# Performance work log

Hardware: AMD Instinct MI355X
Metric: run time of the kernel (lower is better)

## Reference

```python
import jax, jax.numpy as jnp
import numpy as np

N, D, H, C, E = 50000, 128, 4, 32, 600000  # C = D // H
LRELU_SLOPE = 0.2
EPS_LN = 1e-5
EPS_SOFTMAX = 1e-16


def layer_norm(x, g, b):
    m = jnp.mean(x, axis=-1, keepdims=True)
    v = jnp.mean((x - m) ** 2, axis=-1, keepdims=True)
    return (x - m) * jax.lax.rsqrt(v + EPS_LN) * g + b


def setup_inputs() -> dict:
    key = jax.random.key(0)
    ks = jax.random.split(key, 10)
    glorot = lambda k, shape: jax.random.normal(k, shape, jnp.float32) * np.sqrt(2.0 / (shape[0] + shape[-1]))
    return {
        "x": jax.random.normal(ks[0], (N, D), jnp.float32),
        "edge_index": jax.random.randint(ks[1], (2, E), 0, N, jnp.int32),
        "edge_attr": jax.random.uniform(ks[2], (E,), jnp.float32),
        "timestamps": jax.random.uniform(ks[3], (E,), jnp.float32),
        "W_gat": glorot(ks[4], (D, H * C)),
        "att_src": glorot(ks[5], (H, C)),
        "att_dst": glorot(ks[6], (H, C)),
        "bias_gat": jnp.zeros((H * C,), jnp.float32),
        "ln1_g": jnp.ones((D,), jnp.float32),
        "ln1_b": jnp.zeros((D,), jnp.float32),
        "ln2_g": jnp.ones((D,), jnp.float32),
        "ln2_b": jnp.zeros((D,), jnp.float32),
    }


def reference(x, edge_index, edge_attr, timestamps, W_gat, att_src, att_dst,
              bias_gat, ln1_g, ln1_b, ln2_g, ln2_b):
    n = x.shape[0]
    # TemporalAttention is just LayerNorm(x)
    xt = layer_norm(x, ln1_g, ln1_b)

    # GATConv with default add_self_loops=True, concat=True, dropout=0 (eval)
    loop = jnp.arange(n, dtype=edge_index.dtype)
    src = jnp.concatenate([edge_index[0], loop])  # [E+N]
    dst = jnp.concatenate([edge_index[1], loop])  # aggregation target

    h = (xt @ W_gat).reshape(n, H, C)            # [N,H,C]
    a_src = jnp.sum(h * att_src, axis=-1)        # [N,H]
    a_dst = jnp.sum(h * att_dst, axis=-1)        # [N,H]

    alpha = jax.nn.leaky_relu(a_src[src] + a_dst[dst], LRELU_SLOPE)  # [E+N,H]
    amax = jax.ops.segment_max(alpha, dst, num_segments=n)
    alpha = jnp.exp(alpha - amax[dst])
    asum = jax.ops.segment_sum(alpha, dst, num_segments=n)
    alpha = alpha / (asum[dst] + EPS_SOFTMAX)

    msg = h[src] * alpha[:, :, None]             # [E+N,H,C]
    out = jax.ops.segment_sum(msg, dst, num_segments=n).reshape(n, H * C) + bias_gat

    # residual + LayerNorm (dropout is identity in eval)
    return layer_norm(xt + out, ln2_g, ln2_b)
```

## Files before the change

### kernel.cpp

```cpp
#include <hip/hip_runtime.h>
#include <hip/hip_bf16.h>

typedef unsigned short u16;
typedef unsigned int u32;
typedef __attribute__((ext_vector_type(8))) short short8;
typedef __attribute__((ext_vector_type(4))) float f32x4;

#define LRELU_SLOPE 0.2f
#define EPS_LN 1e-5f
#define EPS_SM 1e-16f
#define SCAN_CHUNK 4096
#define NBLK 256

__device__ __forceinline__ float bflo(u32 u){ union{u32 i; float f;} x; x.i = u<<16; return x.f; }
__device__ __forceinline__ float bfhi(u32 u){ union{u32 i; float f;} x; x.i = u & 0xffff0000u; return x.f; }
__device__ __forceinline__ float bf1(u16 u){ union{u32 i; float f;} x; x.i = ((u32)u)<<16; return x.f; }
__device__ __forceinline__ u16 f2bf(float f){
  union{float f; u32 i;} x; x.f=f; u32 i=x.i;
  u32 r = (i + 0x7fffu + ((i>>16)&1u))>>16; return (u16)r;
}
__device__ __forceinline__ u32 pack2(float a, float b){ return (u32)f2bf(a) | ((u32)f2bf(b)<<16); }
__device__ __forceinline__ float lrelu(float x){ return x > 0.f ? x : LRELU_SLOPE*x; }

__device__ __forceinline__ float wsum(float v){
  #pragma unroll
  for(int o=32;o>0;o>>=1) v += __shfl_xor(v,o,64);
  return v;
}

__global__ __launch_bounds__(256) void ln1A_kernel(const float* __restrict__ x,
    const float* __restrict__ g, const float* __restrict__ b,
    u16* __restrict__ xt, int n,
    const int* __restrict__ edst, int* __restrict__ bhT, int E, int CH, int NB){
  __shared__ u32 hist[512];
  int tid = threadIdx.x;
  bool doA = blockIdx.x < NBLK;
  if(doA){ for(int bb=tid; bb<NB; bb+=256) hist[bb]=0u; }

  int row  = blockIdx.x*4 + (tid>>6);
  int lane = tid & 63;
  if(row < n){
    float2 xv = ((const float2*)(x + (size_t)row*128))[lane];
    float v0 = xv.x, v1 = xv.y;
    float mean = wsum(v0+v1) * (1.f/128.f);
    float d0 = v0-mean, d1 = v1-mean;
    float var = wsum(d0*d0 + d1*d1) * (1.f/128.f);
    float rstd = rsqrtf(var + EPS_LN);
    float2 gv = ((const float2*)g)[lane], bv = ((const float2*)b)[lane];
    float o0 = d0*rstd*gv.x + bv.x;
    float o1 = d1*rstd*gv.y + bv.y;
    ((u32*)(xt + (size_t)row*128))[lane] = pack2(o0, o1);
  }
  if(doA){
    __syncthreads();
    int i = blockIdx.x;
    int e0=i*CH, e1=min(E, e0+CH);
    for(int e=e0+tid; e<e1; e+=256) atomicAdd(&hist[(u32)edst[e]>>7], 1u);
    __syncthreads();
    for(int bb=tid; bb<NB; bb+=256) bhT[bb*NBLK + i] = (int)hist[bb];
  }
}

__global__ __launch_bounds__(256) void scanA_kernel(const int* __restrict__ deg,
    int* __restrict__ pref, int* __restrict__ bsum, int n){
  __shared__ int part[256];
  int tid = threadIdx.x;
  int base = blockIdx.x*SCAN_CHUNK + tid*16;
  int v[16]; int s=0;
  #pragma unroll
  for(int i=0;i<16;i++){ int idx=base+i; int xv=(idx<n)? deg[idx]:0; v[i]=s; s+=xv; }
  part[tid]=s; __syncthreads();
  int mys=s;
  for(int off=1;off<256;off<<=1){
    int t = (tid>=off)? part[tid-off] : 0;
    __syncthreads(); part[tid]+=t; __syncthreads();
  }
  int run = part[tid]-mys;
  #pragma unroll
  for(int i=0;i<16;i++){
    int idx=base+i;
    if(idx<=n) pref[idx]=v[i]+run;
  }
  if(tid==255) bsum[blockIdx.x]=part[255];
}

__global__ __launch_bounds__(256) void binC_kernel(const int* __restrict__ src,
    const int* __restrict__ dst, const int* __restrict__ bhpref, const int* __restrict__ bsum2,
    u32* __restrict__ ebuf, int E, int CH, int NB, int nb2){
  __shared__ u32 cur[512];
  __shared__ int boff[64];
  int tid = threadIdx.x, i = blockIdx.x;
  if(tid<64){
    int v = (tid<nb2)? bsum2[tid] : 0;
    int inc = v;
    #pragma unroll
    for(int o=1;o<64;o<<=1){ int t=__shfl_up(inc,o,64); if(tid>=o) inc+=t; }
    boff[tid] = inc - v;
  }
  __syncthreads();
  for(int bb=tid; bb<NB; bb+=256){
    int j = bb*NBLK + i;
    cur[bb] = (u32)(bhpref[j] + boff[j>>12]);
  }
  __syncthreads();
  int e0=i*CH, e1=min(E, e0+CH);
  for(int e=e0+tid; e<e1; e+=256){
    u32 s = (u32)src[e], d = (u32)dst[e];
    u32 pos = atomicAdd(&cur[d>>7], 1u);
    ebuf[pos] = s | ((d & 127u) << 16);
  }
}

__global__ __launch_bounds__(256) void gemmD_kernel(const u16* __restrict__ xt,
    const float* __restrict__ W, const float* __restrict__ att_src, const float* __restrict__ att_dst,
    u16* __restrict__ h, float* __restrict__ a_src, float* __restrict__ a_dst, int n,
    const u32* __restrict__ ebuf, const int* __restrict__ bhpref, const int* __restrict__ bsum2,
    int* __restrict__ rowptr, u16* __restrict__ col, int NB, int nb2, int E){
  __shared__ u16 Wf[16384];
  __shared__ u16 Xb[64*136];
  __shared__ int dcnt[128], dcur[128], dboff[64];
  int tid = threadIdx.x;

  if(blockIdx.x < (u32)NB){
    int bkt = blockIdx.x;
    if(tid<64){
      int v = (tid<nb2)? bsum2[tid] : 0;
      int inc = v;
      #pragma unroll
      for(int o=1;o<64;o<<=1){ int t=__shfl_up(inc,o,64); if(tid>=o) inc+=t; }
      dboff[tid] = inc - v;
    }
    if(tid<128) dcnt[tid]=0;
    __syncthreads();
    int j0 = bkt*NBLK, j1 = (bkt+1)*NBLK;
    int base = bhpref[j0] + dboff[j0>>12];
    int end  = bhpref[j1] + dboff[j1>>12];
    int cb = end - base;
    for(int k=tid; k<cb; k+=256) atomicAdd(&dcnt[(ebuf[base+k]>>16)&127], 1);
    __syncthreads();
    for(int o=1;o<128;o<<=1){
      int t = (tid>=o && tid<128)? dcnt[tid-o] : 0;
      __syncthreads();
      if(tid<128) dcnt[tid]+=t;
      __syncthreads();
    }
    int nd = min(128, n - (bkt<<7));
    if(tid<128){
      int excl = tid? dcnt[tid-1] : 0;
      dcur[tid] = excl;
      if(tid<nd) rowptr[(bkt<<7)+tid] = base + excl;
    }
    if(bkt==0 && tid==0) rowptr[n] = E;
    __syncthreads();
    for(int k=tid; k<cb; k+=256){
      u32 v = ebuf[base+k];
      int l = (int)((v>>16)&127u);
      int p = atomicAdd(&dcur[l], 1);
      col[base+p] = (u16)(v & 0xffffu);
    }
  }

  int r0 = blockIdx.x*64;
  const float4* W4 = (const float4*)W;
  for(int p=tid; p<2048; p+=256){
    int g = p & 31, kk = p >> 5;
    int k0 = kk*2, n0 = g*4;
    float4 w0 = W4[k0*32 + g];
    float4 w1 = W4[(k0+1)*32 + g];
    int ks = k0>>5, q = (k0>>3)&3, j = k0&7;
    float e0[4] = {w0.x,w0.y,w0.z,w0.w};
    float e1[4] = {w1.x,w1.y,w1.z,w1.w};
    #pragma unroll
    for(int u=0;u<4;u++){
      int nn = n0+u;
      int idx = (((nn>>4)*4 + ks)*64 + q*16 + (nn&15))*8 + j;
      ((u32*)Wf)[idx>>1] = pack2(e0[u], e1[u]);
    }
  }
  for(int i=tid; i<1024; i+=256){
    int row = i>>4, seg = i&15;
    int gr = r0+row;
    uint4 v = (gr<n) ? ((const uint4*)(xt + (size_t)gr*128))[seg] : make_uint4(0,0,0,0);
    *(uint4*)&Xb[row*136 + seg*8] = v;
  }
  __syncthreads();

  int w = tid>>6, lane = tid&63;
  int slab = w*16, c = lane&15, q = lane>>4;
  f32x4 acc[8];
  #pragma unroll
  for(int t=0;t<8;t++) acc[t] = (f32x4){0.f,0.f,0.f,0.f};
  #pragma unroll
  for(int ks=0;ks<4;ks++){
    short8 A = *(const short8*)&Xb[(slab + c)*136 + ks*32 + q*8];
    #pragma unroll
    for(int t=0;t<8;t++){
      short8 B = *(const short8*)&Wf[((t*4+ks)*64 + lane)*8];
      acc[t] = __builtin_amdgcn_mfma_f32_16x16x32_bf16(A, B, acc[t], 0, 0, 0);
    }
  }
  __syncthreads();
  #pragma unroll
  for(int t=0;t<8;t++){
    #pragma unroll
    for(int r=0;r<4;r++){
      Xb[(slab + q*4 + r)*136 + t*16 + c] = f2bf(acc[t][r]);
    }
  }
  __syncthreads();
  {
    int row = tid>>2, qt = tid&3;
    int gr = r0+row;
    if(gr<n){
      const uint4* src = (const uint4*)((const char*)Xb + row*272 + qt*64);
      uint4* dst = (uint4*)((char*)(h + (size_t)gr*128) + qt*64);
      dst[0] = src[0];
      dst[1] = src[1];
      dst[2] = src[2];
      dst[3] = src[3];
    }
    int hd = qt;
    if(gr<n){
      float as=0.f, ad=0.f;
      const u16* hp = &Xb[row*136 + hd*32];
      #pragma unroll
      for(int sgm=0;sgm<4;sgm++){
        #pragma unroll
        for(int e=0;e<8;e++){
          float v = bf1(hp[sgm*8+e]);
          as = fmaf(v, att_src[hd*32+sgm*8+e], as);
          ad = fmaf(v, att_dst[hd*32+sgm*8+e], ad);
        }
      }
      a_src[(size_t)gr*4+hd] = as;
      a_dst[(size_t)gr*4+hd] = ad;
    }
  }
}

__global__ __launch_bounds__(256) void agg_kernel(const u16* __restrict__ h,
    const float* __restrict__ a_src, const float* __restrict__ a_dst,
    const int* __restrict__ rowptr, const u16* __restrict__ col,
    const u16* __restrict__ xt, const float* __restrict__ bias,
    const float* __restrict__ g2, const float* __restrict__ b2,
    float* __restrict__ out, int n){
  __shared__ float ybuf[16*68];
  __shared__ int   sxbuf[16*17];
  int lane = threadIdx.x & 63;
  int wv   = threadIdx.x >> 6;
  int g    = lane >> 4;
  int li   = lane & 15;
  int hc   = li >> 2;
  int gid  = wv*4 + g;
  float* yb = ybuf  + gid*68;
  int*   sb = sxbuf + gid*17;
  int d    = blockIdx.x*16 + gid;
  bool dok = d < n;
  int dc   = dok ? d : (n-1);

  float4 ad  = ((const float4*)a_dst)[dc];
  float4 asd = ((const float4*)a_src)[dc];
  float ad_h = hc==0? ad.x  : hc==1? ad.y  : hc==2? ad.z  : ad.w;
  float as_h = hc==0? asd.x : hc==1? asd.y : hc==2? asd.z : asd.w;
  float t_h  = __expf(fminf(lrelu(as_h + ad_h), 60.f));

  int base = rowptr[dc];
  int deg  = dok ? (rowptr[dc+1] - base) : 0;
  int dm = deg;
  dm = max(dm, __shfl_xor(dm, 16, 64));
  dm = max(dm, __shfl_xor(dm, 32, 64));

  float p0=0.f,p1=0.f,p2=0.f,p3=0.f;
  float acc[8]={};
  for(int j0=0;j0<dm;j0+=16){
    int j = j0 + li;
    bool vv = j < deg;
    int sx = vv ? (int)col[base+j] : 0;
    float4 a = ((const float4*)a_src)[sx];
    float y0 = vv ? __expf(fminf(lrelu(a.x+ad.x),60.f)) : 0.f;
    float y1 = vv ? __expf(fminf(lrelu(a.y+ad.y),60.f)) : 0.f;
    float y2 = vv ? __expf(fminf(lrelu(a.z+ad.z),60.f)) : 0.f;
    float y3 = vv ? __expf(fminf(lrelu(a.w+ad.w),60.f)) : 0.f;
    p0+=y0; p1+=y1; p2+=y2; p3+=y3;
    *(float4*)&yb[li*4] = make_float4(y0,y1,y2,y3);
    sb[li] = sx;
    __builtin_amdgcn_sched_barrier(0);
    int ccm = min(deg - j0, 16);
    for(int jj=0; jj<ccm; jj++){
      float al = yb[jj*4 + hc];
      int   sj = sb[jj];
      uint4 hv = *(const uint4*)(h + (size_t)sj*128 + li*8);
      acc[0]=fmaf(al,bflo(hv.x),acc[0]); acc[1]=fmaf(al,bfhi(hv.x),acc[1]);
      acc[2]=fmaf(al,bflo(hv.y),acc[2]); acc[3]=fmaf(al,bfhi(hv.y),acc[3]);
      acc[4]=fmaf(al,bflo(hv.z),acc[4]); acc[5]=fmaf(al,bfhi(hv.z),acc[5]);
      acc[6]=fmaf(al,bflo(hv.w),acc[6]); acc[7]=fmaf(al,bfhi(hv.w),acc[7]);
    }
    __builtin_amdgcn_sched_barrier(0);
  }
  #pragma unroll
  for(int o=1;o<16;o<<=1){
    p0+=__shfl_xor(p0,o,64); p1+=__shfl_xor(p1,o,64);
    p2+=__shfl_xor(p2,o,64); p3+=__shfl_xor(p3,o,64);
  }
  float den = (hc==0? p0 : hc==1? p1 : hc==2? p2 : p3) + t_h + EPS_SM;
  uint4 hd4 = *(const uint4*)(h + (size_t)dc*128 + li*8);
  acc[0]=fmaf(t_h,bflo(hd4.x),acc[0]); acc[1]=fmaf(t_h,bfhi(hd4.x),acc[1]);
  acc[2]=fmaf(t_h,bflo(hd4.y),acc[2]); acc[3]=fmaf(t_h,bfhi(hd4.y),acc[3]);
  acc[4]=fmaf(t_h,bflo(hd4.z),acc[4]); acc[5]=fmaf(t_h,bfhi(hd4.z),acc[5]);
  acc[6]=fmaf(t_h,bflo(hd4.w),acc[6]); acc[7]=fmaf(t_h,bfhi(hd4.w),acc[7]);
  float inv = 1.f/den;

  uint4 xv4 = *(const uint4*)(xt + (size_t)dc*128 + li*8);
  const float* bp = bias + li*8;
  float4 ba = *(const float4*)bp, bb = *(const float4*)(bp+4);
  float r[8];
  r[0]=bflo(xv4.x)+acc[0]*inv+ba.x; r[1]=bfhi(xv4.x)+acc[1]*inv+ba.y;
  r[2]=bflo(xv4.y)+acc[2]*inv+ba.z; r[3]=bfhi(xv4.y)+acc[3]*inv+ba.w;
  r[4]=bflo(xv4.z)+acc[4]*inv+bb.x; r[5]=bfhi(xv4.z)+acc[5]*inv+bb.y;
  r[6]=bflo(xv4.w)+acc[6]*inv+bb.z; r[7]=bfhi(xv4.w)+acc[7]*inv+bb.w;
  float part=0;
  #pragma unroll
  for(int c=0;c<8;c++) part+=r[c];
  #pragma unroll
  for(int o=1;o<16;o<<=1) part += __shfl_xor(part,o,64);
  float mean = part*(1.f/128.f);
  float vp=0;
  #pragma unroll
  for(int c=0;c<8;c++){ float dd=r[c]-mean; vp+=dd*dd; }
  #pragma unroll
  for(int o=1;o<16;o<<=1) vp += __shfl_xor(vp,o,64);
  float var = vp*(1.f/128.f);
  float rstd = rsqrtf(var+EPS_LN);
  const float* gp = g2 + li*8; const float* b2p = b2 + li*8;
  float4 ga = *(const float4*)gp,  gb = *(const float4*)(gp+4);
  float4 c2a= *(const float4*)b2p, c2b= *(const float4*)(b2p+4);
  if(dok){
    float* op = out + (size_t)d*128 + li*8;
    float4 o0 = make_float4((r[0]-mean)*rstd*ga.x+c2a.x, (r[1]-mean)*rstd*ga.y+c2a.y,
                            (r[2]-mean)*rstd*ga.z+c2a.z, (r[3]-mean)*rstd*ga.w+c2a.w);
    float4 o1 = make_float4((r[4]-mean)*rstd*gb.x+c2b.x, (r[5]-mean)*rstd*gb.y+c2b.y,
                            (r[6]-mean)*rstd*gb.z+c2b.z, (r[7]-mean)*rstd*gb.w+c2b.w);
    *(float4*)op     = o0;
    *(float4*)(op+4) = o1;
  }
}

extern "C" void kernel_launch(void* const* d_in, const int* in_sizes, int n_in,
                              void* d_out, int out_size, void* d_ws, size_t ws_size,
                              hipStream_t stream) {
  const float* x     = (const float*)d_in[0];
  const int*   ei    = (const int*)d_in[1];
  const float* W     = (const float*)d_in[4];
  const float* att_s = (const float*)d_in[5];
  const float* att_d = (const float*)d_in[6];
  const float* bias  = (const float*)d_in[7];
  const float* g1    = (const float*)d_in[8];
  const float* b1    = (const float*)d_in[9];
  const float* g2    = (const float*)d_in[10];
  const float* b2    = (const float*)d_in[11];
  int n = in_sizes[0]/128;
  int E = in_sizes[1]/2;
  float* out = (float*)d_out;

  int NB  = (n+127)>>7;
  int CH  = (E + NBLK - 1)/NBLK;
  int NH  = NB*NBLK;
  int nb2 = NH/SCAN_CHUNK + 1;

  char* ws = (char*)d_ws;
  u16*   xt     = (u16*)ws;   ws += (size_t)n*128*2;
  u16*   h      = (u16*)ws;   ws += (size_t)n*128*2;
  float* a_src  = (float*)ws; ws += (size_t)n*4*4;
  float* a_dst  = (float*)ws; ws += (size_t)n*4*4;
  int*   rowptr = (int*)ws;   ws += (((size_t)(n+1)*4 + 255) & ~(size_t)255);
  u16*   col    = (u16*)ws;   ws += (((size_t)E*2 + 255) & ~(size_t)255);
  u32*   ebuf   = (u32*)ws;   ws += (size_t)E*4;
  int*   bhT    = (int*)ws;   ws += (size_t)NH*4;
  int*   bhpref = (int*)ws;   ws += (((size_t)(NH+1)*4 + 255) & ~(size_t)255);
  int*   bsum2  = (int*)ws;   ws += 256*4;

  dim3 b256(256);
  ln1A_kernel <<<(n+3)/4,   b256, 0, stream>>>(x, g1, b1, xt, n, ei+E, bhT, E, CH, NB);
  scanA_kernel<<<nb2,       b256, 0, stream>>>(bhT, bhpref, bsum2, NH);
  binC_kernel <<<NBLK,      b256, 0, stream>>>(ei, ei+E, bhpref, bsum2, ebuf, E, CH, NB, nb2);
  gemmD_kernel<<<(n+63)/64, b256, 0, stream>>>(xt, W, att_s, att_d, h, a_src, a_dst, n,
                                               ebuf, bhpref, bsum2, rowptr, col, NB, nb2, E);
  agg_kernel  <<<(n+15)/16, b256, 0, stream>>>(h, a_src, a_dst, rowptr, col, xt, bias, g2, b2, out, n);
}
```

Before: 175.7 us.

## Merge binning into GEMM launch and fuse per-bucket CSR build into aggregation

The edge-binning pass now runs as extra blocks in the same launch as the feature GEMM, and the per-bucket counting sort that builds col/rowptr moves into the aggregation kernel. Each 512-thread aggregation block owns one 128-node bucket and keeps its row pointers in shared memory. The aim is to drop one kernel launch, remove the global rowptr array, and overlap binning with the GEMM. The aggregation loop also broadcasts edge weights and source indices with wave shuffles instead of shared memory. In exchange, aggregation gets only about 391 large blocks, and each thread handles 4 destinations serially, so parallelism and latency hiding may drop.

Measured after the change: 186.2 us. 1.06x slower.

```diff
diff --git a/kernel.cpp b/kernel.cpp
--- a/kernel.cpp
+++ b/kernel.cpp
@@ -84,83 +84,43 @@
   if(tid==255) bsum[blockIdx.x]=part[255];
 }
 
-__global__ __launch_bounds__(256) void binC_kernel(const int* __restrict__ src,
-    const int* __restrict__ dst, const int* __restrict__ bhpref, const int* __restrict__ bsum2,
+__global__ __launch_bounds__(256) void binCG_kernel(const u16* __restrict__ xt,
+    const float* __restrict__ W, const float* __restrict__ att_src, const float* __restrict__ att_dst,
+    u16* __restrict__ h, float* __restrict__ a_src, float* __restrict__ a_dst, int n,
+    const int* __restrict__ esrc, const int* __restrict__ edst,
+    const int* __restrict__ bhpref, const int* __restrict__ bsum2,
     u32* __restrict__ ebuf, int E, int CH, int NB, int nb2){
+  __shared__ u16 Wf[16384];
+  __shared__ u16 Xb[64*136];
   __shared__ u32 cur[512];
   __shared__ int boff[64];
-  int tid = threadIdx.x, i = blockIdx.x;
-  if(tid<64){
-    int v = (tid<nb2)? bsum2[tid] : 0;
-    int inc = v;
-    #pragma unroll
-    for(int o=1;o<64;o<<=1){ int t=__shfl_up(inc,o,64); if(tid>=o) inc+=t; }
-    boff[tid] = inc - v;
-  }
-  __syncthreads();
-  for(int bb=tid; bb<NB; bb+=256){
-    int j = bb*NBLK + i;
-    cur[bb] = (u32)(bhpref[j] + boff[j>>12]);
-  }
-  __syncthreads();
-  int e0=i*CH, e1=min(E, e0+CH);
-  for(int e=e0+tid; e<e1; e+=256){
-    u32 s = (u32)src[e], d = (u32)dst[e];
-    u32 pos = atomicAdd(&cur[d>>7], 1u);
-    ebuf[pos] = s | ((d & 127u) << 16);
-  }
-}
-
-__global__ __launch_bounds__(256) void gemmD_kernel(const u16* __restrict__ xt,
-    const float* __restrict__ W, const float* __restrict__ att_src, const float* __restrict__ att_dst,
-    u16* __restrict__ h, float* __restrict__ a_src, float* __restrict__ a_dst, int n,
-    const u32* __restrict__ ebuf, const int* __restrict__ bhpref, const int* __restrict__ bsum2,
-    int* __restrict__ rowptr, u16* __restrict__ col, int NB, int nb2, int E){
-  __shared__ u16 Wf[16384];
-  __shared__ u16 Xb[64*136];
-  __shared__ int dcnt[128], dcur[128], dboff[64];
   int tid = threadIdx.x;
 
-  if(blockIdx.x < (u32)NB){
-    int bkt = blockIdx.x;
+  if(blockIdx.x < NBLK){
+    int i = blockIdx.x;
     if(tid<64){
       int v = (tid<nb2)? bsum2[tid] : 0;
       int inc = v;
       #pragma unroll
       for(int o=1;o<64;o<<=1){ int t=__shfl_up(inc,o,64); if(tid>=o) inc+=t; }
-      dboff[tid] = inc - v;
-    }
-    if(tid<128) dcnt[tid]=0;
-    __syncthreads();
-    int j0 = bkt*NBLK, j1 = (bkt+1)*NBLK;
-    int base = bhpref[j0] + dboff[j0>>12];
-    int end  = bhpref[j1] + dboff[j1>>12];
-    int cb = end - base;
-    for(int k=tid; k<cb; k+=256) atomicAdd(&dcnt[(ebuf[base+k]>>16)&127], 1);
-    __syncthreads();
-    for(int o=1;o<128;o<<=1){
-      int t = (tid>=o && tid<128)? dcnt[tid-o] : 0;
-      __syncthreads();
-      if(tid<128) dcnt[tid]+=t;
-      __syncthreads();
-    }
-    int nd = min(128, n - (bkt<<7));
-    if(tid<128){
-      int excl = tid? dcnt[tid-1] : 0;
-      dcur[tid] = excl;
-      if(tid<nd) rowptr[(bkt<<7)+tid] = base + excl;
-    }
-    if(bkt==0 && tid==0) rowptr[n] = E;
-    __syncthreads();
-    for(int k=tid; k<cb; k+=256){
-      u32 v = ebuf[base+k];
-      int l = (int)((v>>16)&127u);
-      int p = atomicAdd(&dcur[l], 1);
-      col[base+p] = (u16)(v & 0xffffu);
-    }
-  }
-
-  int r0 = blockIdx.x*64;
+      boff[tid] = inc - v;
+    }
+    __syncthreads();
+    for(int bb=tid; bb<NB; bb+=256){
+      int j = bb*NBLK + i;
+      cur[bb] = (u32)(bhpref[j] + boff[j>>12]);
+    }
+    __syncthreads();
+    int e0=i*CH, e1=min(E, e0+CH);
+    for(int e=e0+tid; e<e1; e+=256){
+      u32 s = (u32)esrc[e], d = (u32)edst[e];
+      u32 pos = atomicAdd(&cur[d>>7], 1u);
+      ebuf[pos] = s | ((d & 127u) << 16);
+    }
+    return;
+  }
+
+  int r0 = (blockIdx.x - NBLK)*64;
   const float4* W4 = (const float4*)W;
   for(int p=tid; p<2048; p+=256){
     int g = p & 31, kk = p >> 5;
@@ -238,110 +198,152 @@
   }
 }
 
-__global__ __launch_bounds__(256) void agg_kernel(const u16* __restrict__ h,
+__global__ __launch_bounds__(512) void aggD_kernel(const u16* __restrict__ h,
     const float* __restrict__ a_src, const float* __restrict__ a_dst,
-    const int* __restrict__ rowptr, const u16* __restrict__ col,
+    const u32* __restrict__ ebuf, const int* __restrict__ bhpref, const int* __restrict__ bsum2,
+    u16* __restrict__ col,
     const u16* __restrict__ xt, const float* __restrict__ bias,
     const float* __restrict__ g2, const float* __restrict__ b2,
-    float* __restrict__ out, int n){
-  __shared__ float ybuf[16*68];
-  __shared__ int   sxbuf[16*17];
-  int lane = threadIdx.x & 63;
-  int wv   = threadIdx.x >> 6;
+    float* __restrict__ out, int n, int nb2, int E){
+  __shared__ int dcnt[128], dcur[128], dboff[64], lrp[129];
+  int tid = threadIdx.x, bkt = blockIdx.x;
+
+  if(tid<64){
+    int v = (tid<nb2)? bsum2[tid] : 0;
+    int inc = v;
+    #pragma unroll
+    for(int o=1;o<64;o<<=1){ int t=__shfl_up(inc,o,64); if(tid>=o) inc+=t; }
+    dboff[tid] = inc - v;
+  }
+  if(tid<128) dcnt[tid]=0;
+  __syncthreads();
+  int j0 = bkt*NBLK, j1 = j0 + NBLK;
+  int base = bhpref[j0] + dboff[j0>>12];
+  int end  = bhpref[j1] + dboff[j1>>12];
+  int cb = end - base;
+  for(int k=tid; k<cb; k+=512) atomicAdd(&dcnt[(ebuf[base+k]>>16)&127], 1);
+  __syncthreads();
+  for(int o=1;o<128;o<<=1){
+    int t = (tid>=o && tid<128)? dcnt[tid-o] : 0;
+    __syncthreads();
+    if(tid<128) dcnt[tid]+=t;
+    __syncthreads();
+  }
+  if(tid<128){
+    int excl = tid? dcnt[tid-1] : 0;
+    dcur[tid] = excl;
+    lrp[tid]  = base + excl;
+  }
+  if(tid==0) lrp[128] = end;
+  __syncthreads();
+  for(int k=tid; k<cb; k+=512){
+    u32 v = ebuf[base+k];
+    int l = (int)((v>>16)&127u);
+    int p = atomicAdd(&dcur[l], 1);
+    col[base+p] = (u16)(v & 0xffffu);
+  }
+  __syncthreads();
+
+  int lane = tid & 63;
+  int wv   = tid >> 6;
   int g    = lane >> 4;
   int li   = lane & 15;
   int hc   = li >> 2;
-  int gid  = wv*4 + g;
-  float* yb = ybuf  + gid*68;
-  int*   sb = sxbuf + gid*17;
-  int d    = blockIdx.x*16 + gid;
-  bool dok = d < n;
-  int dc   = dok ? d : (n-1);
-
-  float4 ad  = ((const float4*)a_dst)[dc];
-  float4 asd = ((const float4*)a_src)[dc];
-  float ad_h = hc==0? ad.x  : hc==1? ad.y  : hc==2? ad.z  : ad.w;
-  float as_h = hc==0? asd.x : hc==1? asd.y : hc==2? asd.z : asd.w;
-  float t_h  = __expf(fminf(lrelu(as_h + ad_h), 60.f));
-
-  int base = rowptr[dc];
-  int deg  = dok ? (rowptr[dc+1] - base) : 0;
-  int dm = deg;
-  dm = max(dm, __shfl_xor(dm, 16, 64));
-  dm = max(dm, __shfl_xor(dm, 32, 64));
-
-  float p0=0.f,p1=0.f,p2=0.f,p3=0.f;
-  float acc[8]={};
-  for(int j0=0;j0<dm;j0+=16){
-    int j = j0 + li;
-    bool vv = j < deg;
-    int sx = vv ? (int)col[base+j] : 0;
-    float4 a = ((const float4*)a_src)[sx];
-    float y0 = vv ? __expf(fminf(lrelu(a.x+ad.x),60.f)) : 0.f;
-    float y1 = vv ? __expf(fminf(lrelu(a.y+ad.y),60.f)) : 0.f;
-    float y2 = vv ? __expf(fminf(lrelu(a.z+ad.z),60.f)) : 0.f;
-    float y3 = vv ? __expf(fminf(lrelu(a.w+ad.w),60.f)) : 0.f;
-    p0+=y0; p1+=y1; p2+=y2; p3+=y3;
-    *(float4*)&yb[li*4] = make_float4(y0,y1,y2,y3);
-    sb[li] = sx;
-    __builtin_amdgcn_sched_barrier(0);
-    int ccm = min(deg - j0, 16);
-    for(int jj=0; jj<ccm; jj++){
-      float al = yb[jj*4 + hc];
-      int   sj = sb[jj];
-      uint4 hv = *(const uint4*)(h + (size_t)sj*128 + li*8);
-      acc[0]=fmaf(al,bflo(hv.x),acc[0]); acc[1]=fmaf(al,bfhi(hv.x),acc[1]);
-      acc[2]=fmaf(al,bflo(hv.y),acc[2]); acc[3]=fmaf(al,bfhi(hv.y),acc[3]);
-      acc[4]=fmaf(al,bflo(hv.z),acc[4]); acc[5]=fmaf(al,bfhi(hv.z),acc[5]);
-      acc[6]=fmaf(al,bflo(hv.w),acc[6]); acc[7]=fmaf(al,bfhi(hv.w),acc[7]);
-    }
-    __builtin_amdgcn_sched_barrier(0);
-  }
-  #pragma unroll
-  for(int o=1;o<16;o<<=1){
-    p0+=__shfl_xor(p0,o,64); p1+=__shfl_xor(p1,o,64);
-    p2+=__shfl_xor(p2,o,64); p3+=__shfl_xor(p3,o,64);
-  }
-  float den = (hc==0? p0 : hc==1? p1 : hc==2? p2 : p3) + t_h + EPS_SM;
-  uint4 hd4 = *(const uint4*)(h + (size_t)dc*128 + li*8);
-  acc[0]=fmaf(t_h,bflo(hd4.x),acc[0]); acc[1]=fmaf(t_h,bfhi(hd4.x),acc[1]);
-  acc[2]=fmaf(t_h,bflo(hd4.y),acc[2]); acc[3]=fmaf(t_h,bfhi(hd4.y),acc[3]);
-  acc[4]=fmaf(t_h,bflo(hd4.z),acc[4]); acc[5]=fmaf(t_h,bfhi(hd4.z),acc[5]);
-  acc[6]=fmaf(t_h,bflo(hd4.w),acc[6]); acc[7]=fmaf(t_h,bfhi(hd4.w),acc[7]);
-  float inv = 1.f/den;
-
-  uint4 xv4 = *(const uint4*)(xt + (size_t)dc*128 + li*8);
-  const float* bp = bias + li*8;
-  float4 ba = *(const float4*)bp, bb = *(const float4*)(bp+4);
-  float r[8];
-  r[0]=bflo(xv4.x)+acc[0]*inv+ba.x; r[1]=bfhi(xv4.x)+acc[1]*inv+ba.y;
-  r[2]=bflo(xv4.y)+acc[2]*inv+ba.z; r[3]=bfhi(xv4.y)+acc[3]*inv+ba.w;
-  r[4]=bflo(xv4.z)+acc[4]*inv+bb.x; r[5]=bfhi(xv4.z)+acc[5]*inv+bb.y;
-  r[6]=bflo(xv4.w)+acc[6]*inv+bb.z; r[7]=bfhi(xv4.w)+acc[7]*inv+bb.w;
-  float part=0;
-  #pragma unroll
-  for(int c=0;c<8;c++) part+=r[c];
-  #pragma unroll
-  for(int o=1;o<16;o<<=1) part += __shfl_xor(part,o,64);
-  float mean = part*(1.f/128.f);
-  float vp=0;
-  #pragma unroll
-  for(int c=0;c<8;c++){ float dd=r[c]-mean; vp+=dd*dd; }
-  #pragma unroll
-  for(int o=1;o<16;o<<=1) vp += __shfl_xor(vp,o,64);
-  float var = vp*(1.f/128.f);
-  float rstd = rsqrtf(var+EPS_LN);
-  const float* gp = g2 + li*8; const float* b2p = b2 + li*8;
-  float4 ga = *(const float4*)gp,  gb = *(const float4*)(gp+4);
-  float4 c2a= *(const float4*)b2p, c2b= *(const float4*)(b2p+4);
-  if(dok){
-    float* op = out + (size_t)d*128 + li*8;
-    float4 o0 = make_float4((r[0]-mean)*rstd*ga.x+c2a.x, (r[1]-mean)*rstd*ga.y+c2a.y,
-                            (r[2]-mean)*rstd*ga.z+c2a.z, (r[3]-mean)*rstd*ga.w+c2a.w);
-    float4 o1 = make_float4((r[4]-mean)*rstd*gb.x+c2b.x, (r[5]-mean)*rstd*gb.y+c2b.y,
-                            (r[6]-mean)*rstd*gb.z+c2b.z, (r[7]-mean)*rstd*gb.w+c2b.w);
-    *(float4*)op     = o0;
-    *(float4*)(op+4) = o1;
+  int G    = wv*4 + g;
+  int nd   = min(128, n - (bkt<<7));
+  const float4* as4 = (const float4*)a_src;
+  const float4* ad4 = (const float4*)a_dst;
+
+  for(int kk=0; kk<4; kk++){
+    int dl  = G + 32*kk;
+    bool dok = dl < nd;
+    int d   = (bkt<<7) + (dok ? dl : 0);
+    int bd  = lrp[dl];
+    int deg = lrp[dl+1] - bd;
+
+    float4 ad  = ad4[d];
+    float4 asd = as4[d];
+    float ad_h = hc==0? ad.x  : hc==1? ad.y  : hc==2? ad.z  : ad.w;
+    float as_h = hc==0? asd.x : hc==1? asd.y : hc==2? asd.z : asd.w;
+    float t_h  = __expf(fminf(lrelu(as_h + ad_h), 60.f));
+
+    int dm = deg;
+    dm = max(dm, __shfl_xor(dm, 16, 64));
+    dm = max(dm, __shfl_xor(dm, 32, 64));
+
+    float p0=0.f,p1=0.f,p2=0.f,p3=0.f;
+    float acc[8]={};
+    for(int j0e=0;j0e<dm;j0e+=16){
+      int j = j0e + li;
+      bool vv = j < deg;
+      int sx = vv ? (int)col[bd+j] : 0;
+      float4 a = as4[sx];
+      float y0 = vv ? __expf(fminf(lrelu(a.x+ad.x),60.f)) : 0.f;
+      float y1 = vv ? __expf(fminf(lrelu(a.y+ad.y),60.f)) : 0.f;
+      float y2 = vv ? __expf(fminf(lrelu(a.z+ad.z),60.f)) : 0.f;
+      float y3 = vv ? __expf(fminf(lrelu(a.w+ad.w),60.f)) : 0.f;
+      p0+=y0; p1+=y1; p2+=y2; p3+=y3;
+      int ccm = min(deg - j0e, 16);
+      int gbase = g<<4;
+      for(int jj=0; jj<ccm; jj++){
+        int srcl = gbase + jj;
+        float f0=__shfl(y0,srcl,64), f1=__shfl(y1,srcl,64);
+        float f2=__shfl(y2,srcl,64), f3=__shfl(y3,srcl,64);
+        int   sj=__shfl(sx,srcl,64);
+        float al = hc==0? f0 : hc==1? f1 : hc==2? f2 : f3;
+        uint4 hv = *(const uint4*)(h + (size_t)sj*128 + li*8);
+        acc[0]=fmaf(al,bflo(hv.x),acc[0]); acc[1]=fmaf(al,bfhi(hv.x),acc[1]);
+        acc[2]=fmaf(al,bflo(hv.y),acc[2]); acc[3]=fmaf(al,bfhi(hv.y),acc[3]);
+        acc[4]=fmaf(al,bflo(hv.z),acc[4]); acc[5]=fmaf(al,bfhi(hv.z),acc[5]);
+        acc[6]=fmaf(al,bflo(hv.w),acc[6]); acc[7]=fmaf(al,bfhi(hv.w),acc[7]);
+      }
+    }
+    #pragma unroll
+    for(int o=1;o<16;o<<=1){
+      p0+=__shfl_xor(p0,o,64); p1+=__shfl_xor(p1,o,64);
+      p2+=__shfl_xor(p2,o,64); p3+=__shfl_xor(p3,o,64);
+    }
+    float den = (hc==0? p0 : hc==1? p1 : hc==2? p2 : p3) + t_h + EPS_SM;
+    uint4 hd4 = *(const uint4*)(h + (size_t)d*128 + li*8);
+    acc[0]=fmaf(t_h,bflo(hd4.x),acc[0]); acc[1]=fmaf(t_h,bfhi(hd4.x),acc[1]);
+    acc[2]=fmaf(t_h,bflo(hd4.y),acc[2]); acc[3]=fmaf(t_h,bfhi(hd4.y),acc[3]);
+    acc[4]=fmaf(t_h,bflo(hd4.z),acc[4]); acc[5]=fmaf(t_h,bfhi(hd4.z),acc[5]);
+    acc[6]=fmaf(t_h,bflo(hd4.w),acc[6]); acc[7]=fmaf(t_h,bfhi(hd4.w),acc[7]);
+    float inv = 1.f/den;
+
+    uint4 xv4 = *(const uint4*)(xt + (size_t)d*128 + li*8);
+    const float* bp = bias + li*8;
+    float4 ba = *(const float4*)bp, bb = *(const float4*)(bp+4);
+    float r[8];
+    r[0]=bflo(xv4.x)+acc[0]*inv+ba.x; r[1]=bfhi(xv4.x)+acc[1]*inv+ba.y;
+    r[2]=bflo(xv4.y)+acc[2]*inv+ba.z; r[3]=bfhi(xv4.y)+acc[3]*inv+ba.w;
+    r[4]=bflo(xv4.z)+acc[4]*inv+bb.x; r[5]=bfhi(xv4.z)+acc[5]*inv+bb.y;
+    r[6]=bflo(xv4.w)+acc[6]*inv+bb.z; r[7]=bfhi(xv4.w)+acc[7]*inv+bb.w;
+    float part=0;
+    #pragma unroll
+    for(int c=0;c<8;c++) part+=r[c];
+    #pragma unroll
+    for(int o=1;o<16;o<<=1) part += __shfl_xor(part,o,64);
+    float mean = part*(1.f/128.f);
+    float vp=0;
+    #pragma unroll
+    for(int c=0;c<8;c++){ float dd=r[c]-mean; vp+=dd*dd; }
+    #pragma unroll
+    for(int o=1;o<16;o<<=1) vp += __shfl_xor(vp,o,64);
+    float var = vp*(1.f/128.f);
+    float rstd = rsqrtf(var+EPS_LN);
+    const float* gp = g2 + li*8; const float* b2p = b2 + li*8;
+    float4 ga = *(const float4*)gp,  gb = *(const float4*)(gp+4);
+    float4 c2a= *(const float4*)b2p, c2b= *(const float4*)(b2p+4);
+    if(dok){
+      float* op = out + (size_t)d*128 + li*8;
+      float4 o0 = make_float4((r[0]-mean)*rstd*ga.x+c2a.x, (r[1]-mean)*rstd*ga.y+c2a.y,
+                              (r[2]-mean)*rstd*ga.z+c2a.z, (r[3]-mean)*rstd*ga.w+c2a.w);
+      float4 o1 = make_float4((r[4]-mean)*rstd*gb.x+c2b.x, (r[5]-mean)*rstd*gb.y+c2b.y,
+                              (r[6]-mean)*rstd*gb.z+c2b.z, (r[7]-mean)*rstd*gb.w+c2b.w);
+      *(float4*)op     = o0;
+      *(float4*)(op+4) = o1;
+    }
   }
 }
 
@@ -372,18 +374,18 @@
   u16*   h      = (u16*)ws;   ws += (size_t)n*128*2;
   float* a_src  = (float*)ws; ws += (size_t)n*4*4;
   float* a_dst  = (float*)ws; ws += (size_t)n*4*4;
-  int*   rowptr = (int*)ws;   ws += (((size_t)(n+1)*4 + 255) & ~(size_t)255);
   u16*   col    = (u16*)ws;   ws += (((size_t)E*2 + 255) & ~(size_t)255);
   u32*   ebuf   = (u32*)ws;   ws += (size_t)E*4;
   int*   bhT    = (int*)ws;   ws += (size_t)NH*4;
   int*   bhpref = (int*)ws;   ws += (((size_t)(NH+1)*4 + 255) & ~(size_t)255);
   int*   bsum2  = (int*)ws;   ws += 256*4;
 
-  dim3 b256(256);
-  ln1A_kernel <<<(n+3)/4,   b256, 0, stream>>>(x, g1, b1, xt, n, ei+E, bhT, E, CH, NB);
-  scanA_kernel<<<nb2,       b256, 0, stream>>>(bhT, bhpref, bsum2, NH);
-  binC_kernel <<<NBLK,      b256, 0, stream>>>(ei, ei+E, bhpref, bsum2, ebuf, E, CH, NB, nb2);
-  gemmD_kernel<<<(n+63)/64, b256, 0, stream>>>(xt, W, att_s, att_d, h, a_src, a_dst, n,
-                                               ebuf, bhpref, bsum2, rowptr, col, NB, nb2, E);
-  agg_kernel  <<<(n+15)/16, b256, 0, stream>>>(h, a_src, a_dst, rowptr, col, xt, bias, g2, b2, out, n);
-}
+  int gemmTiles = (n+63)/64;
+  dim3 b256(256), b512(512);
+  ln1A_kernel <<<(n+3)/4,        b256, 0, stream>>>(x, g1, b1, xt, n, ei+E, bhT, E, CH, NB);
+  scanA_kernel<<<nb2,            b256, 0, stream>>>(bhT, bhpref, bsum2, NH);
+  binCG_kernel<<<NBLK+gemmTiles, b256, 0, stream>>>(xt, W, att_s, att_d, h, a_src, a_dst, n,
+                                                    ei, ei+E, bhpref, bsum2, ebuf, E, CH, NB, nb2);
+  aggD_kernel <<<NB,             b512, 0, stream>>>(h, a_src, a_dst, ebuf, bhpref, bsum2, col,
+                                                    xt, bias, g2, b2, out, n, nb2, E);
+}
```

## Overlap edge binning with GEMM and use shuffles instead of LDS in aggregation

Applied to the files above, without the earlier changes.

The edge-binning pass (binC) now runs as extra blocks inside the GEMM kernel, so binning overlaps the projection GEMM. The per-bucket CSR build that used to sit inside the GEMM kernel moves to a separate binD kernel launched afterwards. In the aggregation kernel, each lane now computes attention weights for 4 edges of one head, and these are broadcast with wave shuffles instead of being staged through shared memory. This removes the LDS buffers and one barrier-like scheduling fence, at the cost of an extra kernel launch and more shuffle instructions.

New measurement: 180.1 us. +2.5%, slower.

```diff
diff --git a/kernel.cpp b/kernel.cpp
--- a/kernel.cpp
+++ b/kernel.cpp
@@ -84,83 +84,43 @@
   if(tid==255) bsum[blockIdx.x]=part[255];
 }
 
-__global__ __launch_bounds__(256) void binC_kernel(const int* __restrict__ src,
-    const int* __restrict__ dst, const int* __restrict__ bhpref, const int* __restrict__ bsum2,
+__global__ __launch_bounds__(256) void binCG_kernel(const u16* __restrict__ xt,
+    const float* __restrict__ W, const float* __restrict__ att_src, const float* __restrict__ att_dst,
+    u16* __restrict__ h, float* __restrict__ a_src, float* __restrict__ a_dst, int n,
+    const int* __restrict__ esrc, const int* __restrict__ edst,
+    const int* __restrict__ bhpref, const int* __restrict__ bsum2,
     u32* __restrict__ ebuf, int E, int CH, int NB, int nb2){
+  __shared__ u16 Wf[16384];
+  __shared__ u16 Xb[64*136];
   __shared__ u32 cur[512];
   __shared__ int boff[64];
-  int tid = threadIdx.x, i = blockIdx.x;
-  if(tid<64){
-    int v = (tid<nb2)? bsum2[tid] : 0;
-    int inc = v;
-    #pragma unroll
-    for(int o=1;o<64;o<<=1){ int t=__shfl_up(inc,o,64); if(tid>=o) inc+=t; }
-    boff[tid] = inc - v;
-  }
-  __syncthreads();
-  for(int bb=tid; bb<NB; bb+=256){
-    int j = bb*NBLK + i;
-    cur[bb] = (u32)(bhpref[j] + boff[j>>12]);
-  }
-  __syncthreads();
-  int e0=i*CH, e1=min(E, e0+CH);
-  for(int e=e0+tid; e<e1; e+=256){
-    u32 s = (u32)src[e], d = (u32)dst[e];
-    u32 pos = atomicAdd(&cur[d>>7], 1u);
-    ebuf[pos] = s | ((d & 127u) << 16);
-  }
-}
-
-__global__ __launch_bounds__(256) void gemmD_kernel(const u16* __restrict__ xt,
-    const float* __restrict__ W, const float* __restrict__ att_src, const float* __restrict__ att_dst,
-    u16* __restrict__ h, float* __restrict__ a_src, float* __restrict__ a_dst, int n,
-    const u32* __restrict__ ebuf, const int* __restrict__ bhpref, const int* __restrict__ bsum2,
-    int* __restrict__ rowptr, u16* __restrict__ col, int NB, int nb2, int E){
-  __shared__ u16 Wf[16384];
-  __shared__ u16 Xb[64*136];
-  __shared__ int dcnt[128], dcur[128], dboff[64];
   int tid = threadIdx.x;
 
-  if(blockIdx.x < (u32)NB){
-    int bkt = blockIdx.x;
+  if(blockIdx.x < NBLK){
+    int i = blockIdx.x;
     if(tid<64){
       int v = (tid<nb2)? bsum2[tid] : 0;
       int inc = v;
       #pragma unroll
       for(int o=1;o<64;o<<=1){ int t=__shfl_up(inc,o,64); if(tid>=o) inc+=t; }
-      dboff[tid] = inc - v;
-    }
-    if(tid<128) dcnt[tid]=0;
-    __syncthreads();
-    int j0 = bkt*NBLK, j1 = (bkt+1)*NBLK;
-    int base = bhpref[j0] + dboff[j0>>12];
-    int end  = bhpref[j1] + dboff[j1>>12];
-    int cb = end - base;
-    for(int k=tid; k<cb; k+=256) atomicAdd(&dcnt[(ebuf[base+k]>>16)&127], 1);
-    __syncthreads();
-    for(int o=1;o<128;o<<=1){
-      int t = (tid>=o && tid<128)? dcnt[tid-o] : 0;
-      __syncthreads();
-      if(tid<128) dcnt[tid]+=t;
-      __syncthreads();
-    }
-    int nd = min(128, n - (bkt<<7));
-    if(tid<128){
-      int excl = tid? dcnt[tid-1] : 0;
-      dcur[tid] = excl;
-      if(tid<nd) rowptr[(bkt<<7)+tid] = base + excl;
-    }
-    if(bkt==0 && tid==0) rowptr[n] = E;
-    __syncthreads();
-    for(int k=tid; k<cb; k+=256){
-      u32 v = ebuf[base+k];
-      int l = (int)((v>>16)&127u);
-      int p = atomicAdd(&dcur[l], 1);
-      col[base+p] = (u16)(v & 0xffffu);
-    }
-  }
-
-  int r0 = blockIdx.x*64;
+      boff[tid] = inc - v;
+    }
+    __syncthreads();
+    for(int bb=tid; bb<NB; bb+=256){
+      int j = bb*NBLK + i;
+      cur[bb] = (u32)(bhpref[j] + boff[j>>12]);
+    }
+    __syncthreads();
+    int e0=i*CH, e1=min(E, e0+CH);
+    for(int e=e0+tid; e<e1; e+=256){
+      u32 s = (u32)esrc[e], d = (u32)edst[e];
+      u32 pos = atomicAdd(&cur[d>>7], 1u);
+      ebuf[pos] = s | ((d & 127u) << 16);
+    }
+    return;
+  }
+
+  int r0 = (blockIdx.x - NBLK)*64;
   const float4* W4 = (const float4*)W;
   for(int p=tid; p<2048; p+=256){
     int g = p & 31, kk = p >> 5;
@@ -238,30 +198,69 @@
   }
 }
 
+__global__ __launch_bounds__(256) void binD_kernel(const u32* __restrict__ ebuf,
+    const int* __restrict__ bhpref, const int* __restrict__ bsum2,
+    int* __restrict__ rowptr, u16* __restrict__ col, int n, int E, int nb2){
+  __shared__ int cnt[128], cur[128], dboff[64];
+  int tid = threadIdx.x, b = blockIdx.x;
+  if(tid<64){
+    int v = (tid<nb2)? bsum2[tid] : 0;
+    int inc = v;
+    #pragma unroll
+    for(int o=1;o<64;o<<=1){ int t=__shfl_up(inc,o,64); if(tid>=o) inc+=t; }
+    dboff[tid] = inc - v;
+  }
+  if(tid<128) cnt[tid]=0;
+  __syncthreads();
+  int j0 = b*NBLK, j1 = j0 + NBLK;
+  int base = bhpref[j0] + dboff[j0>>12];
+  int end  = bhpref[j1] + dboff[j1>>12];
+  int cb = end - base;
+  for(int k=tid; k<cb; k+=256) atomicAdd(&cnt[(ebuf[base+k]>>16)&127], 1);
+  __syncthreads();
+  for(int o=1;o<128;o<<=1){
+    int t = (tid>=o && tid<128)? cnt[tid-o] : 0;
+    __syncthreads();
+    if(tid<128) cnt[tid]+=t;
+    __syncthreads();
+  }
+  int nd = min(128, n - (b<<7));
+  if(tid<128){
+    int excl = tid? cnt[tid-1] : 0;
+    cur[tid] = excl;
+    if(tid<nd) rowptr[(b<<7)+tid] = base + excl;
+  }
+  if(b==0 && tid==0) rowptr[n] = E;
+  __syncthreads();
+  for(int k=tid; k<cb; k+=256){
+    u32 v = ebuf[base+k];
+    int l = (int)((v>>16)&127u);
+    int p = atomicAdd(&cur[l], 1);
+    col[base+p] = (u16)(v & 0xffffu);
+  }
+}
+
 __global__ __launch_bounds__(256) void agg_kernel(const u16* __restrict__ h,
     const float* __restrict__ a_src, const float* __restrict__ a_dst,
     const int* __restrict__ rowptr, const u16* __restrict__ col,
     const u16* __restrict__ xt, const float* __restrict__ bias,
     const float* __restrict__ g2, const float* __restrict__ b2,
     float* __restrict__ out, int n){
-  __shared__ float ybuf[16*68];
-  __shared__ int   sxbuf[16*17];
   int lane = threadIdx.x & 63;
   int wv   = threadIdx.x >> 6;
   int g    = lane >> 4;
   int li   = lane & 15;
   int hc   = li >> 2;
-  int gid  = wv*4 + g;
-  float* yb = ybuf  + gid*68;
-  int*   sb = sxbuf + gid*17;
-  int d    = blockIdx.x*16 + gid;
+  int eq   = li & 3;
+  int gbase= g << 4;
+  int d    = blockIdx.x*16 + wv*4 + g;
   bool dok = d < n;
   int dc   = dok ? d : (n-1);
 
-  float4 ad  = ((const float4*)a_dst)[dc];
-  float4 asd = ((const float4*)a_src)[dc];
-  float ad_h = hc==0? ad.x  : hc==1? ad.y  : hc==2? ad.z  : ad.w;
-  float as_h = hc==0? asd.x : hc==1? asd.y : hc==2? asd.z : asd.w;
+  float4 ad4v = ((const float4*)a_dst)[dc];
+  float4 as4v = ((const float4*)a_src)[dc];
+  float ad_h = hc==0? ad4v.x : hc==1? ad4v.y : hc==2? ad4v.z : ad4v.w;
+  float as_h = hc==0? as4v.x : hc==1? as4v.y : hc==2? as4v.z : as4v.w;
   float t_h  = __expf(fminf(lrelu(as_h + ad_h), 60.f));
 
   int base = rowptr[dc];
@@ -270,39 +269,46 @@
   dm = max(dm, __shfl_xor(dm, 16, 64));
   dm = max(dm, __shfl_xor(dm, 32, 64));
 
-  float p0=0.f,p1=0.f,p2=0.f,p3=0.f;
+  float psum = 0.f;
   float acc[8]={};
   for(int j0=0;j0<dm;j0+=16){
-    int j = j0 + li;
-    bool vv = j < deg;
-    int sx = vv ? (int)col[base+j] : 0;
-    float4 a = ((const float4*)a_src)[sx];
-    float y0 = vv ? __expf(fminf(lrelu(a.x+ad.x),60.f)) : 0.f;
-    float y1 = vv ? __expf(fminf(lrelu(a.y+ad.y),60.f)) : 0.f;
-    float y2 = vv ? __expf(fminf(lrelu(a.z+ad.z),60.f)) : 0.f;
-    float y3 = vv ? __expf(fminf(lrelu(a.w+ad.w),60.f)) : 0.f;
-    p0+=y0; p1+=y1; p2+=y2; p3+=y3;
-    *(float4*)&yb[li*4] = make_float4(y0,y1,y2,y3);
-    sb[li] = sx;
-    __builtin_amdgcn_sched_barrier(0);
+    int eb = j0 + eq*4;
+    bool v0 = eb+0 < deg, v1 = eb+1 < deg, v2 = eb+2 < deg, v3 = eb+3 < deg;
+    int sx0 = v0 ? (int)col[base+eb+0] : 0;
+    int sx1 = v1 ? (int)col[base+eb+1] : 0;
+    int sx2 = v2 ? (int)col[base+eb+2] : 0;
+    int sx3 = v3 ? (int)col[base+eb+3] : 0;
+    float y0 = v0 ? __expf(fminf(lrelu(a_src[sx0*4+hc]+ad_h),60.f)) : 0.f;
+    float y1 = v1 ? __expf(fminf(lrelu(a_src[sx1*4+hc]+ad_h),60.f)) : 0.f;
+    float y2 = v2 ? __expf(fminf(lrelu(a_src[sx2*4+hc]+ad_h),60.f)) : 0.f;
+    float y3 = v3 ? __expf(fminf(lrelu(a_src[sx3*4+hc]+ad_h),60.f)) : 0.f;
+    psum += (y0+y1) + (y2+y3);
     int ccm = min(deg - j0, 16);
-    for(int jj=0; jj<ccm; jj++){
-      float al = yb[jj*4 + hc];
-      int   sj = sb[jj];
-      uint4 hv = *(const uint4*)(h + (size_t)sj*128 + li*8);
-      acc[0]=fmaf(al,bflo(hv.x),acc[0]); acc[1]=fmaf(al,bfhi(hv.x),acc[1]);
-      acc[2]=fmaf(al,bflo(hv.y),acc[2]); acc[3]=fmaf(al,bfhi(hv.y),acc[3]);
-      acc[4]=fmaf(al,bflo(hv.z),acc[4]); acc[5]=fmaf(al,bfhi(hv.z),acc[5]);
-      acc[6]=fmaf(al,bflo(hv.w),acc[6]); acc[7]=fmaf(al,bfhi(hv.w),acc[7]);
-    }
-    __builtin_amdgcn_sched_barrier(0);
-  }
-  #pragma unroll
-  for(int o=1;o<16;o<<=1){
-    p0+=__shfl_xor(p0,o,64); p1+=__shfl_xor(p1,o,64);
-    p2+=__shfl_xor(p2,o,64); p3+=__shfl_xor(p3,o,64);
-  }
-  float den = (hc==0? p0 : hc==1? p1 : hc==2? p2 : p3) + t_h + EPS_SM;
+    #pragma unroll 1
+    for(int a=0; a<4; a++){
+      int jb = a*4;
+      if(jb >= ccm) break;
+      int srcl = gbase + hc*4 + a;
+      #define AGG_STEP(cc, yv, sv)                                              \
+        if(jb + cc < ccm){                                                      \
+          float al = __shfl(yv, srcl, 64);                                      \
+          int   sj = __shfl(sv, srcl, 64);                                      \
+          uint4 hv = *(const uint4*)(h + (size_t)sj*128 + li*8);                \
+          acc[0]=fmaf(al,bflo(hv.x),acc[0]); acc[1]=fmaf(al,bfhi(hv.x),acc[1]); \
+          acc[2]=fmaf(al,bflo(hv.y),acc[2]); acc[3]=fmaf(al,bfhi(hv.y),acc[3]); \
+          acc[4]=fmaf(al,bflo(hv.z),acc[4]); acc[5]=fmaf(al,bfhi(hv.z),acc[5]); \
+          acc[6]=fmaf(al,bflo(hv.w),acc[6]); acc[7]=fmaf(al,bfhi(hv.w),acc[7]); \
+        }
+      AGG_STEP(0, y0, sx0)
+      AGG_STEP(1, y1, sx1)
+      AGG_STEP(2, y2, sx2)
+      AGG_STEP(3, y3, sx3)
+      #undef AGG_STEP
+    }
+  }
+  psum += __shfl_xor(psum, 1, 64);
+  psum += __shfl_xor(psum, 2, 64);
+  float den = psum + t_h + EPS_SM;
   uint4 hd4 = *(const uint4*)(h + (size_t)dc*128 + li*8);
   acc[0]=fmaf(t_h,bflo(hd4.x),acc[0]); acc[1]=fmaf(t_h,bfhi(hd4.x),acc[1]);
   acc[2]=fmaf(t_h,bflo(hd4.y),acc[2]); acc[3]=fmaf(t_h,bfhi(hd4.y),acc[3]);
@@ -379,11 +385,12 @@
   int*   bhpref = (int*)ws;   ws += (((size_t)(NH+1)*4 + 255) & ~(size_t)255);
   int*   bsum2  = (int*)ws;   ws += 256*4;
 
+  int gemmTiles = (n+63)/64;
   dim3 b256(256);
-  ln1A_kernel <<<(n+3)/4,   b256, 0, stream>>>(x, g1, b1, xt, n, ei+E, bhT, E, CH, NB);
-  scanA_kernel<<<nb2,       b256, 0, stream>>>(bhT, bhpref, bsum2, NH);
-  binC_kernel <<<NBLK,      b256, 0, stream>>>(ei, ei+E, bhpref, bsum2, ebuf, E, CH, NB, nb2);
-  gemmD_kernel<<<(n+63)/64, b256, 0, stream>>>(xt, W, att_s, att_d, h, a_src, a_dst, n,
-                                               ebuf, bhpref, bsum2, rowptr, col, NB, nb2, E);
-  agg_kernel  <<<(n+15)/16, b256, 0, stream>>>(h, a_src, a_dst, rowptr, col, xt, bias, g2, b2, out, n);
-}
+  ln1A_kernel <<<(n+3)/4,        b256, 0, stream>>>(x, g1, b1, xt, n, ei+E, bhT, E, CH, NB);
+  scanA_kernel<<<nb2,            b256, 0, stream>>>(bhT, bhpref, bsum2, NH);
+  binCG_kernel<<<NBLK+gemmTiles, b256, 0, stream>>>(xt, W, att_s, att_d, h, a_src, a_dst, n,
+                                                    ei, ei+E, bhpref, bsum2, ebuf, E, CH, NB, nb2);
+  binD_kernel <<<NB,             b256, 0, stream>>>(ebuf, bhpref, bsum2, rowptr, col, n, E, nb2);
+  agg_kernel  <<<(n+15)/16,      b256, 0, stream>>>(h, a_src, a_dst, rowptr, col, xt, bias, g2, b2, out, n);
+}
```
